# Kernel optimization log

Hardware: AMD Instinct MI355X
Metric: run time of the kernel (lower is better)

The kernel has to match this reference:

```python
import jax, jax.numpy as jnp
import numpy as np

N_BLOCKS = 5
D_HIDDEN = 512
D_LATENT = 512
NUM_FREQ = 10
IMG_H = IMG_W = 128


@jax.custom_vjp
def trunc_exp(x):
    return jnp.exp(x)

def _te_fwd(x):
    return jnp.exp(x), x

def _te_bwd(x, g):
    return (g * jnp.exp(jnp.clip(x, -15.0, 15.0)),)

trunc_exp.defvjp(_te_fwd, _te_bwd)


def setup_inputs() -> dict:
    key = jax.random.key(0)
    ks = jax.random.split(key, 12)
    cam, ray, samp = 2, 1024, 48
    world_xyz = jax.random.normal(ks[0], (cam, ray, samp, 3), jnp.float32) * 0.5
    world_xyz = world_xyz.at[..., 2].add(2.5)  # keep points in front of identity camera
    c2w = jnp.tile(jnp.eye(4, dtype=jnp.float32), (cam, 1, 1))
    k_mat = jnp.tile(jnp.array([[128.0, 0.0, 64.0], [0.0, 128.0, 64.0], [0.0, 0.0, 1.0]], jnp.float32), (cam, 1, 1))
    features = jax.random.normal(ks[1], (cam, D_LATENT, IMG_H, IMG_W), jnp.float32)
    s = 0.02
    d_in = 3 + 3 * 2 * NUM_FREQ  # 63
    return {
        'world_xyz': world_xyz,
        'c2w': c2w,
        'k_mat': k_mat,
        'features': features,
        'lin_in_w': jax.random.normal(ks[2], (d_in, D_HIDDEN), jnp.float32) * s,
        'lin_in_b': jnp.zeros((D_HIDDEN,), jnp.float32),
        'lin_z_w': jax.random.normal(ks[3], (N_BLOCKS, D_LATENT, D_HIDDEN), jnp.float32) * s,
        'lin_z_b': jnp.zeros((N_BLOCKS, D_HIDDEN), jnp.float32),
        'fc0_w': jax.random.normal(ks[4], (N_BLOCKS, D_HIDDEN, D_HIDDEN), jnp.float32) * s,
        'fc0_b': jnp.zeros((N_BLOCKS, D_HIDDEN), jnp.float32),
        'fc1_w': jax.random.normal(ks[5], (N_BLOCKS, D_HIDDEN, D_HIDDEN), jnp.float32) * s,
        'fc1_b': jnp.zeros((N_BLOCKS, D_HIDDEN), jnp.float32),
        'lin_out_w': jax.random.normal(ks[6], (D_HIDDEN, 1), jnp.float32) * s,
        'lin_out_b': jnp.zeros((1,), jnp.float32),
    }


def _bilinear(feat, uv):
    # feat: [C, H, W]; uv: [N, 2] pixel coords. Bilinear, border padding, align_corners=True.
    Hd, Wd = feat.shape[1], feat.shape[2]
    x = jnp.clip(uv[:, 0], 0.0, Wd - 1.0)
    y = jnp.clip(uv[:, 1], 0.0, Hd - 1.0)
    x0 = jnp.floor(x); y0 = jnp.floor(y)
    x0i = x0.astype(jnp.int32); y0i = y0.astype(jnp.int32)
    x1i = jnp.minimum(x0i + 1, Wd - 1); y1i = jnp.minimum(y0i + 1, Hd - 1)
    wx = x - x0; wy = y - y0
    f00 = feat[:, y0i, x0i]; f01 = feat[:, y0i, x1i]
    f10 = feat[:, y1i, x0i]; f11 = feat[:, y1i, x1i]
    out = (f00 * ((1 - wx) * (1 - wy)) + f01 * (wx * (1 - wy)) +
           f10 * ((1 - wx) * wy) + f11 * (wx * wy))
    return out.T  # [N, C]


def _forward(world_xyz, c2w, k_mat, features, lin_in_w, lin_in_b, lin_z_w, lin_z_b,
             fc0_w, fc0_b, fc1_w, fc1_b, lin_out_w, lin_out_b):
    B, R, S, _ = world_xyz.shape
    pts = world_xyz.reshape(B, R * S, 3)
    # world -> camera (w2c = inverse of rigid c2w)
    rot = c2w[:, :3, :3]
    trans = c2w[:, :3, 3]
    cam_xyz = jnp.einsum('bji,bnj->bni', rot, pts - trans[:, None])  # R^T (p - t)
    # project with intrinsics
    uvw = jnp.einsum('bij,bnj->bni', k_mat, cam_xyz)
    z = uvw[..., 2:3]
    z = jnp.where(jnp.abs(z) < 1e-6, 1e-6, z)
    uv = uvw[..., :2] / z  # [B, N, 2] pixel coords
    aligned = jax.vmap(_bilinear)(features, uv)  # [B, N, C]
    # NeRF positional encoding (include_input=True, freqs 2^0..2^9, scaled by 2*pi)
    freqs = 2.0 ** jnp.arange(NUM_FREQ, dtype=jnp.float32)
    scaled = (2.0 * jnp.pi) * cam_xyz[..., None] * freqs  # [B, N, 3, F]
    scaled = scaled.reshape(B, R * S, 3 * NUM_FREQ)
    enc = jnp.concatenate([cam_xyz, jnp.sin(scaled), jnp.cos(scaled)], axis=-1)  # [B, N, 63]
    # ResnetFC: lin_in then residual blocks with latent injection
    h = enc @ lin_in_w + lin_in_b
    for i in range(N_BLOCKS):
        h = h + aligned @ lin_z_w[i] + lin_z_b[i]
        net = jax.nn.relu(h) @ fc0_w[i] + fc0_b[i]
        dx = jax.nn.relu(net) @ fc1_w[i] + fc1_b[i]
        h = h + dx
    sigma = jax.nn.relu(h) @ lin_out_w + lin_out_b  # [B, N, 1]
    return trunc_exp(sigma).reshape(B, R, S, 1)


def reference(world_xyz, c2w, k_mat, features, lin_in_w, lin_in_b, lin_z_w, lin_z_b,
              fc0_w, fc0_b, fc1_w, fc1_b, lin_out_w, lin_out_b):
    return _forward(world_xyz, c2w, k_mat, features, lin_in_w, lin_in_b, lin_z_w, lin_z_b,
                    fc0_w, fc0_b, fc1_w, fc1_b, lin_out_w, lin_out_b)
```

## Files before the change

kernel.cpp:

```cpp
#include <hip/hip_runtime.h>

typedef __bf16 bf16_t;
typedef bf16_t bf16x8 __attribute__((ext_vector_type(8)));
typedef float f32x4 __attribute__((ext_vector_type(4)));
typedef unsigned short u16;

#define P_TOTAL 98304
#define PTS_PER_BATCH 49152

__device__ __forceinline__ u16 f2bs(float f){ bf16_t b=(bf16_t)f; return __builtin_bit_cast(u16,b); }

__device__ __forceinline__ void bar_lds(){
  asm volatile("s_waitcnt lgkmcnt(0)" ::: "memory");
  __builtin_amdgcn_s_barrier();
  __builtin_amdgcn_sched_barrier(0);
}

__device__ __forceinline__ void gload_lds16(const u16* g, u16* l){
  __builtin_amdgcn_global_load_lds((const __attribute__((address_space(1))) void*)g,
                                   (__attribute__((address_space(3))) void*)l, 16, 0, 0);
}

__global__ void k_wtrans15(const float* __restrict__ lz, const float* __restrict__ f0,
                           const float* __restrict__ f1, u16* __restrict__ dst){
  int kt = blockIdx.x, ns = blockIdx.y, z = blockIdx.z;
  const float* src = (z<5) ? (lz + (size_t)z*262144)
                   : (z<10 ? (f0 + (size_t)(z-5)*262144)
                           : (f1 + (size_t)(z-10)*262144));
  u16* d = dst + (size_t)z*262144 + (size_t)(ns*16 + kt)*1024;
  int l = threadIdx.x;
  int col = ns*32 + (l&15);
  int kr  = kt*32 + (l>>4)*8;
  #pragma unroll
  for (int nt=0;nt<2;nt++){
    bf16x8 o;
    #pragma unroll
    for (int j=0;j<8;j++) o[j] = (bf16_t)src[(size_t)(kr+j)*512 + col + nt*16];
    *(bf16x8*)(d + nt*512 + l*8) = o;
  }
}

__global__ void k_wtrans_in(const float* __restrict__ w, u16* __restrict__ dst){
  int kt = blockIdx.x, ns = blockIdx.y;
  u16* d = dst + (size_t)(ns*2 + kt)*1024;
  int l = threadIdx.x;
  int col = ns*32 + (l&15);
  int kr  = kt*32 + (l>>4)*8;
  #pragma unroll
  for (int nt=0;nt<2;nt++){
    bf16x8 o;
    #pragma unroll
    for (int j=0;j<8;j++){
      int k = kr + j;
      o[j] = (k < 63) ? (bf16_t)w[(size_t)k*512 + col + nt*16] : (bf16_t)0.f;
    }
    *(bf16x8*)(d + nt*512 + l*8) = o;
  }
}

__global__ void k_featT(const float* __restrict__ feat, u16* __restrict__ featT){
  int x = threadIdx.x;
  int c8 = blockIdx.x*8;
  int y = blockIdx.y, b = blockIdx.z;
  float v[8];
  #pragma unroll
  for (int j=0;j<8;j++)
    v[j] = feat[(((size_t)(b*512 + c8 + j))*128 + y)*128 + x];
  bf16x8 o;
  #pragma unroll
  for (int j=0;j<8;j++) o[j] = (bf16_t)v[j];
  *(bf16x8*)(featT + (((size_t)(b*128 + y))*128 + x)*512 + c8) = o;
}

__global__ __launch_bounds__(1024) void k_points(
    const float* __restrict__ world, const float* __restrict__ c2w,
    const float* __restrict__ kmat, const u16* __restrict__ featT,
    u16* __restrict__ alignedF, u16* __restrict__ encF){
  __shared__ u16 act[16*520];
  __shared__ u16 encs[16*72];
  int wid = threadIdx.x >> 6, lane = threadIdx.x & 63;
  int p0 = blockIdx.x*16;
  int gp = p0 + wid;
  int b = gp / PTS_PER_BATCH;
  const float* wp = world + (size_t)gp*3;
  float px = wp[0], py = wp[1], pz = wp[2];
  const float* cw = c2w + b*16;
  float dx = px - cw[3], dy = py - cw[7], dz = pz - cw[11];
  float cx = cw[0]*dx + cw[4]*dy + cw[8]*dz;
  float cy = cw[1]*dx + cw[5]*dy + cw[9]*dz;
  float cz = cw[2]*dx + cw[6]*dy + cw[10]*dz;
  const float* km = kmat + b*9;
  float u0 = km[0]*cx + km[1]*cy + km[2]*cz;
  float v0 = km[3]*cx + km[4]*cy + km[5]*cz;
  float zz = km[6]*cx + km[7]*cy + km[8]*cz;
  if (fabsf(zz) < 1e-6f) zz = 1e-6f;
  float uu = u0/zz, vv = v0/zz;
  float xf = fminf(fmaxf(uu, 0.f), 127.f);
  float yf = fminf(fmaxf(vv, 0.f), 127.f);
  float x0f = floorf(xf), y0f = floorf(yf);
  int x0 = (int)x0f, y0 = (int)y0f;
  int x1 = min(x0+1,127), y1 = min(y0+1,127);
  float wx = xf - x0f, wy = yf - y0f;
  float w00 = (1.f-wx)*(1.f-wy), w01 = wx*(1.f-wy), w10 = (1.f-wx)*wy, w11 = wx*wy;
  size_t fb = (size_t)b*128*128*512;
  int c8 = lane*8;
  const bf16x8 t00 = *(const bf16x8*)(featT + fb + (size_t)(y0*128+x0)*512 + c8);
  const bf16x8 t01 = *(const bf16x8*)(featT + fb + (size_t)(y0*128+x1)*512 + c8);
  const bf16x8 t10 = *(const bf16x8*)(featT + fb + (size_t)(y1*128+x0)*512 + c8);
  const bf16x8 t11 = *(const bf16x8*)(featT + fb + (size_t)(y1*128+x1)*512 + c8);
  bf16x8 o;
  #pragma unroll
  for (int j=0;j<8;j++){
    float r = (float)t00[j]*w00 + (float)t01[j]*w01 + (float)t10[j]*w10 + (float)t11[j]*w11;
    o[j] = (bf16_t)r;
  }
  *(bf16x8*)&act[wid*520 + lane*8] = o;
  float cam[3] = {cx, cy, cz};
  float e;
  if (lane < 3) e = cam[lane];
  else if (lane < 33){
    int i = (lane-3)/10, f = (lane-3)%10;
    e = sinf(6.2831855f * cam[i] * (float)(1<<f));
  } else if (lane < 63){
    int i = (lane-33)/10, f = (lane-33)%10;
    e = cosf(6.2831855f * cam[i] * (float)(1<<f));
  } else e = 0.f;
  encs[wid*72 + lane] = f2bs(e);
  __syncthreads();
  int t = threadIdx.x;
  int g = blockIdx.x & 3;
  size_t blk = (size_t)(blockIdx.x >> 2);
  {
    int kt = t>>6, lo = t&63, fm = lo&15, fk8 = lo>>4;
    bf16x8 v = *(const bf16x8*)&act[fm*520 + kt*32 + fk8*8];
    *(bf16x8*)(alignedF + blk*32768 + (size_t)(kt*4+g)*512 + lo*8) = v;
  }
  if (t < 128){
    int kt = t>>6, lo = t&63, fm = lo&15, fk8 = lo>>4;
    bf16x8 v = *(const bf16x8*)&encs[fm*72 + kt*32 + fk8*8];
    *(bf16x8*)(encF + blk*4096 + (size_t)(kt*4+g)*512 + lo*8) = v;
  }
}


#define MFMA_BF16(A,B,C) __builtin_amdgcn_mfma_f32_16x16x32_bf16(A,B,C,0,0,0)

__device__ __forceinline__ void mfma_cluster(const bf16x8& a0, const bf16x8& a1,
                                             const bf16x8 (&br)[4], f32x4 (&acc)[4][2]){
  __builtin_amdgcn_s_setprio(1);
  #pragma unroll
  for (int q=0;q<4;q++){
    acc[q][0] = MFMA_BF16(a0, br[q], acc[q][0]);
    acc[q][1] = MFMA_BF16(a1, br[q], acc[q][1]);
  }
  __builtin_amdgcn_s_setprio(0);
}

template<int NK>
__device__ __forceinline__ void gemm6(const u16* bp, const u16* __restrict__ apS,
                                      const u16* __restrict__ apN,
                                      f32x4 (&acc)[4][2], bf16x8 (&a)[2][2]){
  #pragma unroll 1
  for (int kb=0; kb<NK/2-1; ++kb){
    const u16* bk = bp  + kb*4096;
    const u16* ak = apS + kb*2048;
    {
      bf16x8 br[4];
      #pragma unroll
      for (int q=0;q<4;q++) br[q] = *(const bf16x8*)(bk + q*512);
      mfma_cluster(a[0][0], a[0][1], br, acc);
      a[0][0] = *(const bf16x8*)(ak + 2048);
      a[0][1] = *(const bf16x8*)(ak + 2048 + 512);
    }
    {
      bf16x8 br[4];
      #pragma unroll
      for (int q=0;q<4;q++) br[q] = *(const bf16x8*)(bk + 2048 + q*512);
      mfma_cluster(a[1][0], a[1][1], br, acc);
      a[1][0] = *(const bf16x8*)(ak + 3072);
      a[1][1] = *(const bf16x8*)(ak + 3072 + 512);
    }
  }
  {
    const u16* bk = bp + (NK/2-1)*4096;
    {
      bf16x8 br[4];
      #pragma unroll
      for (int q=0;q<4;q++) br[q] = *(const bf16x8*)(bk + q*512);
      mfma_cluster(a[0][0], a[0][1], br, acc);
      a[0][0] = *(const bf16x8*)(apN);
      a[0][1] = *(const bf16x8*)(apN + 512);
    }
    {
      bf16x8 br[4];
      #pragma unroll
      for (int q=0;q<4;q++) br[q] = *(const bf16x8*)(bk + 2048 + q*512);
      mfma_cluster(a[1][0], a[1][1], br, acc);
      a[1][0] = *(const bf16x8*)(apN + 1024);
      a[1][1] = *(const bf16x8*)(apN + 1536);
    }
  }
}

__device__ __forceinline__ void add_bias4(const float* __restrict__ bias, int wn32, int rq,
                                          f32x4 (&acc)[4][2]){
  #pragma unroll
  for (int nt=0; nt<2; ++nt){
    f32x4 bv = *(const f32x4*)&bias[wn32 + nt*16 + rq];
    #pragma unroll
    for (int bt=0; bt<4; ++bt)
      #pragma unroll
      for (int r=0; r<4; ++r)
        acc[bt][nt][r] += bv[r];
  }
}

__device__ __forceinline__ void write_relu4(u16* dst, int w, int fm, int fk8,
                                            f32x4 (&acc)[4][2]){
  u16* base = dst + w*2048 + (fk8>>1)*128 + fm*8 + (fk8&1)*4;
  #pragma unroll
  for (int bt=0; bt<4; ++bt)
    #pragma unroll
    for (int nt=0; nt<2; ++nt){
      u16 p0 = f2bs(fmaxf(acc[bt][nt][0], 0.f));
      u16 p1 = f2bs(fmaxf(acc[bt][nt][1], 0.f));
      u16 p2 = f2bs(fmaxf(acc[bt][nt][2], 0.f));
      u16 p3 = f2bs(fmaxf(acc[bt][nt][3], 0.f));
      uint2 v;
      v.x = (unsigned)p0 | ((unsigned)p1 << 16);
      v.y = (unsigned)p2 | ((unsigned)p3 << 16);
      *(uint2*)(base + bt*512 + nt*256) = v;
    }
}

__global__ __launch_bounds__(1024, 4) void k_net(
    const u16* __restrict__ alignedF, const u16* __restrict__ encF,
    const u16* __restrict__ wtin, const float* __restrict__ b_in,
    const u16* __restrict__ wts, const float* __restrict__ bz,
    const float* __restrict__ b0, const float* __restrict__ b1,
    const float* __restrict__ wout, const float* __restrict__ bout,
    float* __restrict__ out)
{
  __shared__ u16 bufA[32768];
  __shared__ u16 bufB[32768];
  const int t = threadIdx.x, w = t>>6, l = t&63;
  const int fm = l&15, fk8 = l>>4, rq = fk8*4;
  const int wn32 = w*32;

  {
    const u16* srcA = alignedF + (size_t)blockIdx.x*32768;
    #pragma unroll
    for (int j=0;j<4;j++)
      gload_lds16(srcA + j*8192 + t*8, bufA + j*8192 + t*8);
    if (t < 512){
      const u16* srcE = encF + (size_t)blockIdx.x*4096;
      gload_lds16(srcE + t*8, bufB + t*8);
    }
  }
  asm volatile("s_waitcnt vmcnt(0)" ::: "memory");
  __builtin_amdgcn_s_barrier();
  __builtin_amdgcn_sched_barrier(0);

  const u16* apEl = wtin + (size_t)w*2048 + l*8;
  bf16x8 a[2][2];
  a[0][0] = *(const bf16x8*)(apEl);        a[0][1] = *(const bf16x8*)(apEl + 512);
  a[1][0] = *(const bf16x8*)(apEl + 1024); a[1][1] = *(const bf16x8*)(apEl + 1536);

  f32x4 h[4][2] = {};
  gemm6<2>(bufB + l*8, apEl, wts + (size_t)w*16384 + l*8, h, a);
  add_bias4(b_in, wn32, rq, h);

  #pragma unroll 1
  for (int i=0;i<5;i++){
    const u16* apz  = wts + (size_t)i*262144      + (size_t)w*16384 + l*8;
    const u16* apf0 = wts + (size_t)(5+i)*262144  + (size_t)w*16384 + l*8;
    const u16* apf1 = wts + (size_t)(10+i)*262144 + (size_t)w*16384 + l*8;
    const u16* apzn = (i<4) ? (wts + (size_t)(i+1)*262144 + (size_t)w*16384 + l*8) : apEl;

    gemm6<16>(bufA + l*8, apz, apf0, h, a);
    add_bias4(bz + i*512, wn32, rq, h);
    bar_lds();
    write_relu4(bufB, w, fm, fk8, h);
    bar_lds();
    f32x4 acc[4][2] = {};
    gemm6<16>(bufB + l*8, apf0, apf1, acc, a);
    add_bias4(b0 + i*512, wn32, rq, acc);
    bar_lds();
    write_relu4(bufB, w, fm, fk8, acc);
    bar_lds();
    gemm6<16>(bufB + l*8, apf1, apzn, h, a);
    add_bias4(b1 + i*512, wn32, rq, h);
  }

  float s[4];
  {
    #pragma unroll
    for (int bt=0; bt<4; ++bt) s[bt] = 0.f;
    #pragma unroll
    for (int nt=0; nt<2; ++nt){
      f32x4 wv = *(const f32x4*)&wout[wn32 + nt*16 + rq];
      #pragma unroll
      for (int bt=0; bt<4; ++bt)
        #pragma unroll
        for (int r=0; r<4; ++r)
          s[bt] += fmaxf(h[bt][nt][r], 0.f) * wv[r];
    }
  }
  #pragma unroll
  for (int bt=0; bt<4; ++bt){
    s[bt] += __shfl_xor(s[bt], 16, 64);
    s[bt] += __shfl_xor(s[bt], 32, 64);
  }
  bar_lds();
  float* red = (float*)bufB;
  if (l < 16){
    #pragma unroll
    for (int bt=0; bt<4; ++bt)
      red[w*64 + bt*16 + l] = s[bt];
  }
  bar_lds();
  if (t < 64){
    float aa = bout[0];
    #pragma unroll
    for (int wv=0; wv<16; wv++) aa += red[wv*64 + t];
    out[blockIdx.x*64 + t] = expf(aa);
  }
}

extern "C" void kernel_launch(void* const* d_in, const int* in_sizes, int n_in,
                              void* d_out, int out_size, void* d_ws, size_t ws_size,
                              hipStream_t stream) {
  const float* world = (const float*)d_in[0];
  const float* c2w   = (const float*)d_in[1];
  const float* kmat  = (const float*)d_in[2];
  const float* feat  = (const float*)d_in[3];
  const float* w_in  = (const float*)d_in[4];
  const float* b_in  = (const float*)d_in[5];
  const float* w_z   = (const float*)d_in[6];
  const float* b_z   = (const float*)d_in[7];
  const float* w_f0  = (const float*)d_in[8];
  const float* b_f0  = (const float*)d_in[9];
  const float* w_f1  = (const float*)d_in[10];
  const float* b_f1  = (const float*)d_in[11];
  const float* w_out = (const float*)d_in[12];
  const float* b_out = (const float*)d_in[13];
  float* out = (float*)d_out;
  char* ws = (char*)d_ws;

  size_t off = 0;
  u16* wts   = (u16*)(ws + off); off += (size_t)15*262144*2;
  u16* wtin  = (u16*)(ws + off); off += (size_t)512*64*2;
  u16* featT = (u16*)(ws + off); off += (size_t)2*128*128*512*2;
  u16* alignedF = (u16*)(ws + off); off += (size_t)P_TOTAL*512*2;
  u16* encF  = (u16*)(ws + off); off += (size_t)P_TOTAL*64*2;

  k_wtrans15<<<dim3(16,16,15), 64, 0, stream>>>(w_z, w_f0, w_f1, wts);
  k_wtrans_in<<<dim3(2,16,1), 64, 0, stream>>>(w_in, wtin);
  k_featT<<<dim3(64,128,2), 128, 0, stream>>>(feat, featT);
  k_points<<<dim3(P_TOTAL/16), 1024, 0, stream>>>(world, c2w, kmat, featT, alignedF, encF);
  k_net<<<dim3(P_TOTAL/64), 1024, 0, stream>>>(alignedF, encF, wtin, b_in, wts,
      b_z, b_f0, b_f1, w_out, b_out, out);
}
```

Before: 834.3 us.

## Make MLP kernel persistent with prefetch of next tile; merge prep kernels

The three preprocessing kernels (weight transposes and feature transpose) are merged into one launch to cut launch overhead. The network kernel becomes persistent with 256 blocks, each looping over 6 tiles of 64 points. During the last residual block it prefetches the next tile's latent and encoding rows into LDS, overlapping that load with compute. A separate LDS buffer holds the encoding. The cost is that with 1024 threads and 4 blocks per CU, 256 blocks may fill the 256 CUs only about one block deep, which lowers occupancy and loses the latency hiding that many resident blocks gave.

```diff
diff --git a/kernel.cpp b/kernel.cpp
--- a/kernel.cpp
+++ b/kernel.cpp
@@ -7,6 +7,8 @@
 
 #define P_TOTAL 98304
 #define PTS_PER_BATCH 49152
+#define NTILE 1536
+#define NBLK 256
 
 __device__ __forceinline__ u16 f2bs(float f){ bf16_t b=(bf16_t)f; return __builtin_bit_cast(u16,b); }
 
@@ -16,60 +18,72 @@
   __builtin_amdgcn_sched_barrier(0);
 }
 
+__device__ __forceinline__ void bar_vm(){
+  asm volatile("s_waitcnt vmcnt(0) lgkmcnt(0)" ::: "memory");
+  __builtin_amdgcn_s_barrier();
+  __builtin_amdgcn_sched_barrier(0);
+}
+
 __device__ __forceinline__ void gload_lds16(const u16* g, u16* l){
   __builtin_amdgcn_global_load_lds((const __attribute__((address_space(1))) void*)g,
                                    (__attribute__((address_space(3))) void*)l, 16, 0, 0);
 }
 
-__global__ void k_wtrans15(const float* __restrict__ lz, const float* __restrict__ f0,
-                           const float* __restrict__ f1, u16* __restrict__ dst){
-  int kt = blockIdx.x, ns = blockIdx.y, z = blockIdx.z;
-  const float* src = (z<5) ? (lz + (size_t)z*262144)
-                   : (z<10 ? (f0 + (size_t)(z-5)*262144)
-                           : (f1 + (size_t)(z-10)*262144));
-  u16* d = dst + (size_t)z*262144 + (size_t)(ns*16 + kt)*1024;
-  int l = threadIdx.x;
-  int col = ns*32 + (l&15);
-  int kr  = kt*32 + (l>>4)*8;
-  #pragma unroll
-  for (int nt=0;nt<2;nt++){
+__global__ void k_prep(const float* __restrict__ feat, u16* __restrict__ featT,
+                       const float* __restrict__ lz, const float* __restrict__ f0,
+                       const float* __restrict__ f1, u16* __restrict__ wts,
+                       const float* __restrict__ w_in, u16* __restrict__ wtin){
+  int blk = blockIdx.x, t = threadIdx.x;
+  if (blk < 16384){
+    int c8 = (blk & 63)*8;
+    int y  = (blk >> 6) & 127;
+    int b  = blk >> 13;
+    int x  = t;
+    float v[8];
+    #pragma unroll
+    for (int j=0;j<8;j++)
+      v[j] = feat[(((size_t)(b*512 + c8 + j))*128 + y)*128 + x];
     bf16x8 o;
     #pragma unroll
-    for (int j=0;j<8;j++) o[j] = (bf16_t)src[(size_t)(kr+j)*512 + col + nt*16];
-    *(bf16x8*)(d + nt*512 + l*8) = o;
-  }
-}
-
-__global__ void k_wtrans_in(const float* __restrict__ w, u16* __restrict__ dst){
-  int kt = blockIdx.x, ns = blockIdx.y;
-  u16* d = dst + (size_t)(ns*2 + kt)*1024;
-  int l = threadIdx.x;
-  int col = ns*32 + (l&15);
-  int kr  = kt*32 + (l>>4)*8;
-  #pragma unroll
-  for (int nt=0;nt<2;nt++){
-    bf16x8 o;
-    #pragma unroll
-    for (int j=0;j<8;j++){
-      int k = kr + j;
-      o[j] = (k < 63) ? (bf16_t)w[(size_t)k*512 + col + nt*16] : (bf16_t)0.f;
-    }
-    *(bf16x8*)(d + nt*512 + l*8) = o;
-  }
-}
-
-__global__ void k_featT(const float* __restrict__ feat, u16* __restrict__ featT){
-  int x = threadIdx.x;
-  int c8 = blockIdx.x*8;
-  int y = blockIdx.y, b = blockIdx.z;
-  float v[8];
-  #pragma unroll
-  for (int j=0;j<8;j++)
-    v[j] = feat[(((size_t)(b*512 + c8 + j))*128 + y)*128 + x];
-  bf16x8 o;
-  #pragma unroll
-  for (int j=0;j<8;j++) o[j] = (bf16_t)v[j];
-  *(bf16x8*)(featT + (((size_t)(b*128 + y))*128 + x)*512 + c8) = o;
+    for (int j=0;j<8;j++) o[j] = (bf16_t)v[j];
+    *(bf16x8*)(featT + (((size_t)(b*128 + y))*128 + x)*512 + c8) = o;
+  } else if (blk < 20224){
+    if (t < 64){
+      int idx = blk - 16384;
+      int kt = idx & 15, ns = (idx>>4) & 15, z = idx >> 8;
+      const float* src = (z<5) ? (lz + (size_t)z*262144)
+                       : (z<10 ? (f0 + (size_t)(z-5)*262144)
+                               : (f1 + (size_t)(z-10)*262144));
+      u16* d = wts + (size_t)z*262144 + (size_t)(ns*16 + kt)*1024;
+      int col = ns*32 + (t&15);
+      int kr  = kt*32 + (t>>4)*8;
+      #pragma unroll
+      for (int nt=0;nt<2;nt++){
+        bf16x8 o;
+        #pragma unroll
+        for (int j=0;j<8;j++) o[j] = (bf16_t)src[(size_t)(kr+j)*512 + col + nt*16];
+        *(bf16x8*)(d + nt*512 + t*8) = o;
+      }
+    }
+  } else {
+    if (t < 64){
+      int idx = blk - 20224;
+      int kt = idx & 1, ns = idx >> 1;
+      u16* d = wtin + (size_t)(ns*2 + kt)*1024;
+      int col = ns*32 + (t&15);
+      int kr  = kt*32 + (t>>4)*8;
+      #pragma unroll
+      for (int nt=0;nt<2;nt++){
+        bf16x8 o;
+        #pragma unroll
+        for (int j=0;j<8;j++){
+          int k = kr + j;
+          o[j] = (k < 63) ? (bf16_t)w_in[(size_t)k*512 + col + nt*16] : (bf16_t)0.f;
+        }
+        *(bf16x8*)(d + nt*512 + t*8) = o;
+      }
+    }
+  }
 }
 
 __global__ __launch_bounds__(1024) void k_points(
@@ -243,87 +257,101 @@
 {
   __shared__ u16 bufA[32768];
   __shared__ u16 bufB[32768];
+  __shared__ u16 bufE[4096];
   const int t = threadIdx.x, w = t>>6, l = t&63;
   const int fm = l&15, fk8 = l>>4, rq = fk8*4;
   const int wn32 = w*32;
 
+  int tid = blockIdx.x;
+
   {
-    const u16* srcA = alignedF + (size_t)blockIdx.x*32768;
+    const u16* srcA = alignedF + (size_t)tid*32768;
     #pragma unroll
     for (int j=0;j<4;j++)
       gload_lds16(srcA + j*8192 + t*8, bufA + j*8192 + t*8);
-    if (t < 512){
-      const u16* srcE = encF + (size_t)blockIdx.x*4096;
-      gload_lds16(srcE + t*8, bufB + t*8);
-    }
-  }
-  asm volatile("s_waitcnt vmcnt(0)" ::: "memory");
-  __builtin_amdgcn_s_barrier();
-  __builtin_amdgcn_sched_barrier(0);
+    if (t < 512)
+      gload_lds16(encF + (size_t)tid*4096 + t*8, bufE + t*8);
+  }
 
   const u16* apEl = wtin + (size_t)w*2048 + l*8;
+  const u16* apz0 = wts + (size_t)w*16384 + l*8;
   bf16x8 a[2][2];
   a[0][0] = *(const bf16x8*)(apEl);        a[0][1] = *(const bf16x8*)(apEl + 512);
   a[1][0] = *(const bf16x8*)(apEl + 1024); a[1][1] = *(const bf16x8*)(apEl + 1536);
 
-  f32x4 h[4][2] = {};
-  gemm6<2>(bufB + l*8, apEl, wts + (size_t)w*16384 + l*8, h, a);
-  add_bias4(b_in, wn32, rq, h);
+  bar_vm();
 
   #pragma unroll 1
-  for (int i=0;i<5;i++){
-    const u16* apz  = wts + (size_t)i*262144      + (size_t)w*16384 + l*8;
-    const u16* apf0 = wts + (size_t)(5+i)*262144  + (size_t)w*16384 + l*8;
-    const u16* apf1 = wts + (size_t)(10+i)*262144 + (size_t)w*16384 + l*8;
-    const u16* apzn = (i<4) ? (wts + (size_t)(i+1)*262144 + (size_t)w*16384 + l*8) : apEl;
-
-    gemm6<16>(bufA + l*8, apz, apf0, h, a);
-    add_bias4(bz + i*512, wn32, rq, h);
+  for (int tile=0; tile<NTILE/NBLK; ++tile){
+    f32x4 h[4][2] = {};
+    gemm6<2>(bufE + l*8, apEl, apz0, h, a);
+    add_bias4(b_in, wn32, rq, h);
+
+    #pragma unroll 1
+    for (int i=0;i<5;i++){
+      const u16* apz  = wts + (size_t)i*262144      + (size_t)w*16384 + l*8;
+      const u16* apf0 = wts + (size_t)(5+i)*262144  + (size_t)w*16384 + l*8;
+      const u16* apf1 = wts + (size_t)(10+i)*262144 + (size_t)w*16384 + l*8;
+      const u16* apzn = (i<4) ? (wts + (size_t)(i+1)*262144 + (size_t)w*16384 + l*8) : apEl;
+
+      gemm6<16>(bufA + l*8, apz, apf0, h, a);
+      add_bias4(bz + i*512, wn32, rq, h);
+      bar_lds();
+      if (i == 4 && tile < NTILE/NBLK - 1){
+        const u16* srcA = alignedF + (size_t)(tid + NBLK)*32768;
+        #pragma unroll
+        for (int j=0;j<4;j++)
+          gload_lds16(srcA + j*8192 + t*8, bufA + j*8192 + t*8);
+        if (t < 512)
+          gload_lds16(encF + (size_t)(tid + NBLK)*4096 + t*8, bufE + t*8);
+      }
+      write_relu4(bufB, w, fm, fk8, h);
+      bar_lds();
+      f32x4 acc[4][2] = {};
+      gemm6<16>(bufB + l*8, apf0, apf1, acc, a);
+      add_bias4(b0 + i*512, wn32, rq, acc);
+      bar_lds();
+      write_relu4(bufB, w, fm, fk8, acc);
+      bar_lds();
+      gemm6<16>(bufB + l*8, apf1, apzn, h, a);
+      add_bias4(b1 + i*512, wn32, rq, h);
+    }
+
+    float s[4];
+    {
+      #pragma unroll
+      for (int bt=0; bt<4; ++bt) s[bt] = 0.f;
+      #pragma unroll
+      for (int nt=0; nt<2; ++nt){
+        f32x4 wv = *(const f32x4*)&wout[wn32 + nt*16 + rq];
+        #pragma unroll
+        for (int bt=0; bt<4; ++bt)
+          #pragma unroll
+          for (int r=0; r<4; ++r)
+            s[bt] += fmaxf(h[bt][nt][r], 0.f) * wv[r];
+      }
+    }
+    #pragma unroll
+    for (int bt=0; bt<4; ++bt){
+      s[bt] += __shfl_xor(s[bt], 16, 64);
+      s[bt] += __shfl_xor(s[bt], 32, 64);
+    }
     bar_lds();
-    write_relu4(bufB, w, fm, fk8, h);
+    float* red = (float*)bufB;
+    if (l < 16){
+      #pragma unroll
+      for (int bt=0; bt<4; ++bt)
+        red[w*64 + bt*16 + l] = s[bt];
+    }
     bar_lds();
-    f32x4 acc[4][2] = {};
-    gemm6<16>(bufB + l*8, apf0, apf1, acc, a);
-    add_bias4(b0 + i*512, wn32, rq, acc);
-    bar_lds();
-    write_relu4(bufB, w, fm, fk8, acc);
-    bar_lds();
-    gemm6<16>(bufB + l*8, apf1, apzn, h, a);
-    add_bias4(b1 + i*512, wn32, rq, h);
-  }
-
-  float s[4];
-  {
-    #pragma unroll
-    for (int bt=0; bt<4; ++bt) s[bt] = 0.f;
-    #pragma unroll
-    for (int nt=0; nt<2; ++nt){
-      f32x4 wv = *(const f32x4*)&wout[wn32 + nt*16 + rq];
-      #pragma unroll
-      for (int bt=0; bt<4; ++bt)
-        #pragma unroll
-        for (int r=0; r<4; ++r)
-          s[bt] += fmaxf(h[bt][nt][r], 0.f) * wv[r];
-    }
-  }
-  #pragma unroll
-  for (int bt=0; bt<4; ++bt){
-    s[bt] += __shfl_xor(s[bt], 16, 64);
-    s[bt] += __shfl_xor(s[bt], 32, 64);
-  }
-  bar_lds();
-  float* red = (float*)bufB;
-  if (l < 16){
-    #pragma unroll
-    for (int bt=0; bt<4; ++bt)
-      red[w*64 + bt*16 + l] = s[bt];
-  }
-  bar_lds();
-  if (t < 64){
-    float aa = bout[0];
-    #pragma unroll
-    for (int wv=0; wv<16; wv++) aa += red[wv*64 + t];
-    out[blockIdx.x*64 + t] = expf(aa);
+    if (t < 64){
+      float aa = bout[0];
+      #pragma unroll
+      for (int wv=0; wv<16; wv++) aa += red[wv*64 + t];
+      out[tid*64 + t] = expf(aa);
+    }
+    tid += NBLK;
+    bar_vm();
   }
 }
 
@@ -354,10 +382,8 @@
   u16* alignedF = (u16*)(ws + off); off += (size_t)P_TOTAL*512*2;
   u16* encF  = (u16*)(ws + off); off += (size_t)P_TOTAL*64*2;
 
-  k_wtrans15<<<dim3(16,16,15), 64, 0, stream>>>(w_z, w_f0, w_f1, wts);
-  k_wtrans_in<<<dim3(2,16,1), 64, 0, stream>>>(w_in, wtin);
-  k_featT<<<dim3(64,128,2), 128, 0, stream>>>(feat, featT);
+  k_prep<<<dim3(20256), 128, 0, stream>>>(feat, featT, w_z, w_f0, w_f1, wts, w_in, wtin);
   k_points<<<dim3(P_TOTAL/16), 1024, 0, stream>>>(world, c2w, kmat, featT, alignedF, encF);
-  k_net<<<dim3(P_TOTAL/64), 1024, 0, stream>>>(alignedF, encF, wtin, b_in, wts,
+  k_net<<<dim3(NBLK), 1024, 0, stream>>>(alignedF, encF, wtin, b_in, wts,
       b_z, b_f0, b_f1, w_out, b_out, out);
 }
```

New measurement: 858.4 us. +2.9%, slower.
